# Performance work log

Measured on AMD Instinct MI355X. Metric: run time of the kernel, lower is better.

Reference implementation:

```python
import jax, jax.numpy as jnp
import numpy as np
import math

NUM_HEADS = 16
SIZE = 1024
HEAD_SIZE = SIZE // NUM_HEADS
B, S = 2, 2048


def setup_inputs() -> dict:
    key = jax.random.key(0)
    ks = jax.random.split(key, 11)
    sc = 1.0 / math.sqrt(SIZE)
    inp = {
        "q": jax.random.normal(ks[0], (B, S, SIZE), dtype=jnp.float32),
        "k": jax.random.normal(ks[1], (B, S, SIZE), dtype=jnp.float32),
        "v": jax.random.normal(ks[2], (B, S, SIZE), dtype=jnp.float32),
        "Wq": jax.random.normal(ks[3], (SIZE, SIZE), dtype=jnp.float32) * sc,
        "bq": jax.random.normal(ks[4], (SIZE,), dtype=jnp.float32) * sc,
        "Wk": jax.random.normal(ks[5], (SIZE, SIZE), dtype=jnp.float32) * sc,
        "bk": jax.random.normal(ks[6], (SIZE,), dtype=jnp.float32) * sc,
        "Wv": jax.random.normal(ks[7], (SIZE, SIZE), dtype=jnp.float32) * sc,
        "bv": jax.random.normal(ks[8], (SIZE,), dtype=jnp.float32) * sc,
        "Wo": jax.random.normal(ks[9], (SIZE, SIZE), dtype=jnp.float32) * sc,
        "bo": jax.random.normal(ks[10], (SIZE,), dtype=jnp.float32) * sc,
    }
    return inp


def _split_heads(x):
    # [B, S, SIZE] -> [B, H, S, D]
    b, s, _ = x.shape
    return x.reshape(b, s, NUM_HEADS, HEAD_SIZE).transpose(0, 2, 1, 3)


def reference(q, k, v, Wq, bq, Wk, bk, Wv, bv, Wo, bo):
    qh = _split_heads(q @ Wq.T + bq) / math.sqrt(HEAD_SIZE)  # [B,H,S,D]
    kh = _split_heads(k @ Wk.T + bk)
    vh = _split_heads(v @ Wv.T + bv)
    scores = jnp.einsum("bhqd,bhkd->bhqk", qh, kh)  # [B,H,S,S]
    attn = jax.nn.softmax(scores, axis=-1)
    ctx = jnp.einsum("bhqk,bhkd->bhqd", attn, vh)  # [B,H,S,D]
    ctx = ctx.transpose(0, 2, 1, 3).reshape(q.shape[0], -1, SIZE)
    return ctx @ Wo.T + bo
```

## Files before the change

### kernel.cpp

```cpp
#include <hip/hip_runtime.h>
#include <hip/hip_bf16.h>

#define SIZE 1024
#define NH 16
#define HD 64
#define BB 2
#define SS 2048
#define MROWS (BB * SS)
#define QT 256
#define NQT (SS / QT)
#define NKT ((SS / 2) / 64)

using bf16 = __hip_bfloat16;
using frag16 = __attribute__((ext_vector_type(8))) short;
using f32x4 = __attribute__((ext_vector_type(4))) float;
typedef unsigned int u32;

__device__ __forceinline__ void glds16(const bf16* g, bf16* l) {
    __builtin_amdgcn_global_load_lds(
        (const __attribute__((address_space(1))) u32*)g,
        (__attribute__((address_space(3))) u32*)l, 16, 0, 0);
}

__device__ __forceinline__ void cvt_store8(bf16* dst, const float* src) {
    float4 a = *(const float4*)src;
    float4 b = *(const float4*)(src + 4);
    bf16 t[8];
    t[0] = __float2bfloat16(a.x); t[1] = __float2bfloat16(a.y);
    t[2] = __float2bfloat16(a.z); t[3] = __float2bfloat16(a.w);
    t[4] = __float2bfloat16(b.x); t[5] = __float2bfloat16(b.y);
    t[6] = __float2bfloat16(b.z); t[7] = __float2bfloat16(b.w);
    *(uint4*)dst = *(const uint4*)t;
}

__global__ __launch_bounds__(256) void cast_kernel(
    const float* __restrict__ Wq, const float* __restrict__ Wk,
    const float* __restrict__ Wv, const float* __restrict__ Wo,
    const float* __restrict__ q, const float* __restrict__ k,
    const float* __restrict__ v,
    bf16* __restrict__ Wb, bf16* __restrict__ qb,
    bf16* __restrict__ kb, bf16* __restrict__ vb)
{
    const int z = blockIdx.z;
    const float* s; bf16* d; int n;
    switch (z) {
        case 0: s = Wq; d = Wb;                   n = SIZE * SIZE;  break;
        case 1: s = Wk; d = Wb + SIZE * SIZE;     n = SIZE * SIZE;  break;
        case 2: s = Wv; d = Wb + 2 * SIZE * SIZE; n = SIZE * SIZE;  break;
        case 3: s = Wo; d = Wb + 3 * SIZE * SIZE; n = SIZE * SIZE;  break;
        case 4: s = q;  d = qb;                   n = MROWS * SIZE; break;
        case 5: s = k;  d = kb;                   n = MROWS * SIZE; break;
        default: s = v; d = vb;                   n = MROWS * SIZE; break;
    }
    const int i = (blockIdx.x * 256 + threadIdx.x) * 8;
    if (i < n) cvt_store8(d + i, s + i);
}

__device__ __forceinline__ void gemm_body(
    const bf16* __restrict__ X, const bf16* __restrict__ W,
    const float* __restrict__ bias, bf16* __restrict__ Y, float scale, bool vt_mode)
{
    __shared__ __align__(16) bf16 smem[8704];
    bf16* As = smem;
    bf16* Bs = smem + 4096;

    const int tid = threadIdx.x;
    const int wave = tid >> 6;
    const int lane = tid & 63;
    const int lane15 = lane & 15;
    const int quad = lane >> 4;
    const int bm = blockIdx.y * 128;
    const int bn = blockIdx.x * 128;
    const int wm = (wave & 1) * 64;
    const int wn = (wave >> 1) * 64;

    f32x4 acc[4][4];
#pragma unroll
    for (int i = 0; i < 4; i++)
#pragma unroll
        for (int j = 0; j < 4; j++)
            acc[i][j] = (f32x4){0.f, 0.f, 0.f, 0.f};

    const int srow = lane >> 2;
    const int scol = (lane & 3) * 8;

    for (int kt = 0; kt < SIZE / 32; kt++) {
        const int k0 = kt * 32;
        __syncthreads();
#pragma unroll
        for (int n = 0; n < 2; n++) {
            const int c = wave * 2 + n;
            glds16(X + (size_t)(bm + c * 16 + srow) * SIZE + k0 + scol, As + c * 512);
            glds16(W + (size_t)(bn + c * 16 + srow) * SIZE + k0 + scol, Bs + c * 512);
        }
        __syncthreads();

        frag16 a[4], b[4];
#pragma unroll
        for (int mi = 0; mi < 4; mi++)
            a[mi] = *(const frag16*)(As + (wm + mi * 16 + lane15) * 32 + quad * 8);
#pragma unroll
        for (int ni = 0; ni < 4; ni++)
            b[ni] = *(const frag16*)(Bs + (wn + ni * 16 + lane15) * 32 + quad * 8);
#pragma unroll
        for (int mi = 0; mi < 4; mi++)
#pragma unroll
            for (int ni = 0; ni < 4; ni++)
                acc[mi][ni] = __builtin_amdgcn_mfma_f32_16x16x32_bf16(
                    a[mi], b[ni], acc[mi][ni], 0, 0, 0);
    }

    if (!vt_mode) {
#pragma unroll
        for (int ni = 0; ni < 4; ni++) {
            const int col = bn + wn + ni * 16 + lane15;
            const float bv = bias[col];
#pragma unroll
            for (int mi = 0; mi < 4; mi++) {
                const int row = bm + wm + mi * 16 + quad * 4;
#pragma unroll
                for (int r = 0; r < 4; r++)
                    Y[(size_t)(row + r) * SIZE + col] =
                        __float2bfloat16((acc[mi][ni][r] + bv) * scale);
            }
        }
    } else {
        bf16* tr = smem;
        const int bloc = bm >> 11;
        const int s0g = bm & (SS - 1);
#pragma unroll
        for (int p = 0; p < 2; p++) {
            __syncthreads();
            if ((wave >> 1) == p) {
#pragma unroll
                for (int ni = 0; ni < 4; ni++) {
                    const int colp = ni * 16 + lane15;
                    const float bv = bias[bn + p * 64 + colp];
#pragma unroll
                    for (int mi = 0; mi < 4; mi++) {
                        const int row = wm + mi * 16 + quad * 4;
#pragma unroll
                        for (int r = 0; r < 4; r++)
                            tr[colp * 136 + row + r] =
                                __float2bfloat16(acc[mi][ni][r] + bv);
                    }
                }
            }
            __syncthreads();
            const int colp = tid >> 2;
            const int gcol = bn + p * 64 + colp;
            const int hh = gcol >> 6, dd = gcol & (HD - 1);
            bf16* dst = (bf16*)Y + ((size_t)(bloc * NH + hh) * HD + dd) * SS
                        + s0g + (tid & 3) * 32;
            const bf16* src = tr + colp * 136 + (tid & 3) * 32;
#pragma unroll
            for (int j = 0; j < 4; j++)
                *(uint4*)(dst + j * 8) = *(const uint4*)(src + j * 8);
        }
    }
}

__global__ __launch_bounds__(256) void qkv_proj_kernel(
    const bf16* __restrict__ qb, const bf16* __restrict__ kb, const bf16* __restrict__ vb,
    const bf16* __restrict__ Wb,
    const float* __restrict__ bq, const float* __restrict__ bk, const float* __restrict__ bv,
    bf16* __restrict__ qh, bf16* __restrict__ kh, bf16* __restrict__ vt)
{
    const bf16 *X, *W; const float* bi; bf16* Y; float sc; bool vm;
    if (blockIdx.z == 0)      { X = qb; W = Wb;                   bi = bq; Y = qh; sc = 0.125f; vm = false; }
    else if (blockIdx.z == 1) { X = kb; W = Wb + SIZE * SIZE;     bi = bk; Y = kh; sc = 1.0f;   vm = false; }
    else                      { X = vb; W = Wb + 2 * SIZE * SIZE; bi = bv; Y = vt; sc = 1.0f;   vm = true;  }
    gemm_body(X, W, bi, Y, sc, vm);
}

__global__ __launch_bounds__(256) void attn_kernel(
    const bf16* __restrict__ qh, const bf16* __restrict__ kh,
    const bf16* __restrict__ vt, bf16* __restrict__ po, float* __restrict__ pl)
{
    __shared__ __align__(16) bf16 Ks[2][64][72];
    __shared__ __align__(16) bf16 Vs[2][64][72];
    __shared__ __align__(16) bf16 Ps[4][64][72];

    const int tid = threadIdx.x;
    const int wave = tid >> 6;
    const int lane = tid & 63;
    const int lane15 = lane & 15;
    const int quad = lane >> 4;

    const int b = blockIdx.z, h = blockIdx.y;
    const int qt = blockIdx.x >> 1;
    const int sh = blockIdx.x & 1;
    const int q0 = qt * QT;

    const size_t baseq = (size_t)b * SS * SIZE + (size_t)h * HD;
    const size_t basev = (size_t)(b * NH + h) * HD * SS;
    const float LOG2E = 1.44269504088896340736f;
    const float OFF = 12.0f * LOG2E;

    frag16 aq[4][2];
#pragma unroll
    for (int m = 0; m < 4; m++) {
        const int qrow = q0 + wave * 64 + m * 16 + lane15;
        const bf16* qp = qh + baseq + (size_t)qrow * SIZE + quad * 8;
        aq[m][0] = *(const frag16*)(qp);
        aq[m][1] = *(const frag16*)(qp + 32);
    }

    frag16 bones;
#pragma unroll
    for (int e = 0; e < 8; e++) bones[e] = (short)0x3F80;

    f32x4 ofrag[4][4], l_frag[4];
#pragma unroll
    for (int m = 0; m < 4; m++) {
        l_frag[m] = (f32x4){0.f, 0.f, 0.f, 0.f};
#pragma unroll
        for (int dt = 0; dt < 4; dt++) ofrag[m][dt] = (f32x4){0.f, 0.f, 0.f, 0.f};
    }

    const int sr = tid >> 3;
    const int sc = (tid & 7) * 8;

    uint4 rk0, rk1, rv0, rv1;

#define ISSUE(KT)                                                              \
    {                                                                          \
        const int s0_ = sh * (SS / 2) + (KT) * 64;                             \
        rk0 = *(const uint4*)(kh + baseq + (size_t)(s0_ + sr) * SIZE + sc);    \
        rk1 = *(const uint4*)(kh + baseq + (size_t)(s0_ + sr + 32) * SIZE + sc);\
        rv0 = *(const uint4*)(vt + basev + (size_t)sr * SS + s0_ + sc);        \
        rv1 = *(const uint4*)(vt + basev + (size_t)(sr + 32) * SS + s0_ + sc); \
    }
#define COMMIT(BUF)                                                            \
    {                                                                          \
        *(uint4*)&Ks[BUF][sr][sc] = rk0; *(uint4*)&Ks[BUF][sr + 32][sc] = rk1; \
        *(uint4*)&Vs[BUF][sr][sc] = rv0; *(uint4*)&Vs[BUF][sr + 32][sc] = rv1; \
    }

    ISSUE(0); COMMIT(0);
    __syncthreads();

    for (int kt = 0; kt < NKT; kt++) {
        const int buf = kt & 1;
        if (kt + 1 < NKT) ISSUE(kt + 1);
        __builtin_amdgcn_sched_barrier(0);

        frag16 kf[4][2];
#pragma unroll
        for (int nt = 0; nt < 4; nt++) {
            kf[nt][0] = *(const frag16*)&Ks[buf][nt * 16 + lane15][quad * 8];
            kf[nt][1] = *(const frag16*)&Ks[buf][nt * 16 + lane15][32 + quad * 8];
        }
#pragma unroll
        for (int m = 0; m < 4; m++) {
#pragma unroll
            for (int nt = 0; nt < 4; nt++) {
                f32x4 c = (f32x4){0.f, 0.f, 0.f, 0.f};
                c = __builtin_amdgcn_mfma_f32_16x16x32_bf16(kf[nt][0], aq[m][0], c, 0, 0, 0);
                c = __builtin_amdgcn_mfma_f32_16x16x32_bf16(kf[nt][1], aq[m][1], c, 0, 0, 0);
                bf16 p4[4];
#pragma unroll
                for (int r = 0; r < 4; r++)
                    p4[r] = __float2bfloat16(exp2f(c[r] * LOG2E - OFF));
                *(uint2*)&Ps[wave][m * 16 + lane15][nt * 16 + quad * 4] = *(const uint2*)p4;
            }
        }
        __builtin_amdgcn_wave_barrier();

        frag16 ap[4][2];
#pragma unroll
        for (int m = 0; m < 4; m++)
#pragma unroll
            for (int c2 = 0; c2 < 2; c2++)
                ap[m][c2] = *(const frag16*)&Ps[wave][m * 16 + lane15][c2 * 32 + quad * 8];

        __builtin_amdgcn_s_setprio(1);
#pragma unroll
        for (int m = 0; m < 4; m++)
#pragma unroll
            for (int c2 = 0; c2 < 2; c2++)
                l_frag[m] = __builtin_amdgcn_mfma_f32_16x16x32_bf16(
                    ap[m][c2], bones, l_frag[m], 0, 0, 0);

#pragma unroll
        for (int dt = 0; dt < 4; dt++) {
            frag16 bv0 = *(const frag16*)&Vs[buf][dt * 16 + lane15][quad * 8];
            frag16 bv1 = *(const frag16*)&Vs[buf][dt * 16 + lane15][32 + quad * 8];
#pragma unroll
            for (int m = 0; m < 4; m++) {
                ofrag[m][dt] = __builtin_amdgcn_mfma_f32_16x16x32_bf16(ap[m][0], bv0, ofrag[m][dt], 0, 0, 0);
                ofrag[m][dt] = __builtin_amdgcn_mfma_f32_16x16x32_bf16(ap[m][1], bv1, ofrag[m][dt], 0, 0, 0);
            }
        }
        __builtin_amdgcn_s_setprio(0);

        if (kt + 1 < NKT) {
            COMMIT(buf ^ 1);
            __syncthreads();
        }
    }
#undef ISSUE
#undef COMMIT

    const int pb = ((b * NH + h) * NQT + qt) * 2 + sh;
    if (lane15 == 0) {
        float* plp = pl + (size_t)pb * QT;
#pragma unroll
        for (int m = 0; m < 4; m++)
#pragma unroll
            for (int r = 0; r < 4; r++)
                plp[wave * 64 + m * 16 + quad * 4 + r] = l_frag[m][r];
    }
    bf16* pop = po + (size_t)pb * QT * HD;
#pragma unroll
    for (int m = 0; m < 4; m++)
#pragma unroll
        for (int dt = 0; dt < 4; dt++)
#pragma unroll
            for (int r = 0; r < 4; r++)
                pop[(size_t)(wave * 64 + m * 16 + quad * 4 + r) * HD + dt * 16 + lane15] =
                    __float2bfloat16(ofrag[m][dt][r]);
}

__global__ __launch_bounds__(256) void combine_kernel(
    const bf16* __restrict__ po, const float* __restrict__ pl, bf16* __restrict__ ctx)
{
    const int b = blockIdx.z, h = blockIdx.y, qt = blockIdx.x;
    const int t = (b * NH + h) * NQT + (qt >> 1);
    const int rbase = (qt & 1) * 128;
    const bf16* p0 = po + (size_t)(t * 2 + 0) * QT * HD;
    const bf16* p1 = po + (size_t)(t * 2 + 1) * QT * HD;
    const int qr = threadIdx.x >> 1;
    const int dh = (threadIdx.x & 1) * 32;
    const int row = rbase + qr;
    const float l = pl[(size_t)(t * 2) * QT + row] + pl[(size_t)(t * 2 + 1) * QT + row];
    const float inv = 1.0f / fmaxf(l, 1e-30f);
    bf16* dst = ctx + ((size_t)b * SS + qt * 128 + qr) * SIZE + h * HD + dh;
    const bf16* s0p = p0 + row * HD + dh;
    const bf16* s1p = p1 + row * HD + dh;
#pragma unroll
    for (int j = 0; j < 32; j += 8) {
        uint4 u0 = *(const uint4*)(s0p + j);
        uint4 u1 = *(const uint4*)(s1p + j);
        const bf16* a = (const bf16*)&u0;
        const bf16* bt = (const bf16*)&u1;
        bf16 o[8];
#pragma unroll
        for (int e = 0; e < 8; e++)
            o[e] = __float2bfloat16((__bfloat162float(a[e]) + __bfloat162float(bt[e])) * inv);
        *(uint4*)(dst + j) = *(const uint4*)o;
    }
}

__global__ __launch_bounds__(256) void out_proj_kernel(
    const bf16* __restrict__ ctx, const bf16* __restrict__ Wob,
    const float* __restrict__ bo, float* __restrict__ out)
{
    __shared__ __align__(16) bf16 As[64 * 32];
    __shared__ __align__(16) bf16 Bs[128 * 32];

    const int tid = threadIdx.x;
    const int wave = tid >> 6;
    const int lane = tid & 63;
    const int lane15 = lane & 15;
    const int quad = lane >> 4;
    const int bm = blockIdx.y * 64;
    const int bn = blockIdx.x * 128;
    const int wn = wave * 32;

    f32x4 acc[4][2];
#pragma unroll
    for (int i = 0; i < 4; i++)
#pragma unroll
        for (int j = 0; j < 2; j++)
            acc[i][j] = (f32x4){0.f, 0.f, 0.f, 0.f};

    const int srow = lane >> 2;
    const int scol = (lane & 3) * 8;

    for (int kt = 0; kt < SIZE / 32; kt++) {
        const int k0 = kt * 32;
        __syncthreads();
        glds16(ctx + (size_t)(bm + wave * 16 + srow) * SIZE + k0 + scol, As + wave * 512);
#pragma unroll
        for (int n = 0; n < 2; n++) {
            const int c = wave * 2 + n;
            glds16(Wob + (size_t)(bn + c * 16 + srow) * SIZE + k0 + scol, Bs + c * 512);
        }
        __syncthreads();

        frag16 a[4], b[2];
#pragma unroll
        for (int mi = 0; mi < 4; mi++)
            a[mi] = *(const frag16*)(As + (mi * 16 + lane15) * 32 + quad * 8);
#pragma unroll
        for (int ni = 0; ni < 2; ni++)
            b[ni] = *(const frag16*)(Bs + (wn + ni * 16 + lane15) * 32 + quad * 8);
#pragma unroll
        for (int mi = 0; mi < 4; mi++)
#pragma unroll
            for (int ni = 0; ni < 2; ni++)
                acc[mi][ni] = __builtin_amdgcn_mfma_f32_16x16x32_bf16(
                    a[mi], b[ni], acc[mi][ni], 0, 0, 0);
    }

#pragma unroll
    for (int ni = 0; ni < 2; ni++) {
        const int col = bn + wn + ni * 16 + lane15;
        const float bv = bo[col];
#pragma unroll
        for (int mi = 0; mi < 4; mi++) {
            const int row = bm + mi * 16 + quad * 4;
#pragma unroll
            for (int r = 0; r < 4; r++)
                out[(size_t)(row + r) * SIZE + col] = acc[mi][ni][r] + bv;
        }
    }
}

extern "C" void kernel_launch(void* const* d_in, const int* in_sizes, int n_in,
                              void* d_out, int out_size, void* d_ws, size_t ws_size,
                              hipStream_t stream) {
    const float* q  = (const float*)d_in[0];
    const float* k  = (const float*)d_in[1];
    const float* v  = (const float*)d_in[2];
    const float* Wq = (const float*)d_in[3];
    const float* bq = (const float*)d_in[4];
    const float* Wk = (const float*)d_in[5];
    const float* bk = (const float*)d_in[6];
    const float* Wv = (const float*)d_in[7];
    const float* bv = (const float*)d_in[8];
    const float* Wo = (const float*)d_in[9];
    const float* bo = (const float*)d_in[10];
    float* out = (float*)d_out;

    bf16* Wb  = (bf16*)d_ws;
    bf16* qb  = Wb + (size_t)4 * SIZE * SIZE;
    bf16* kb  = qb + (size_t)MROWS * SIZE;
    bf16* vb  = kb + (size_t)MROWS * SIZE;
    bf16* qh  = vb + (size_t)MROWS * SIZE;
    bf16* kh  = qh + (size_t)MROWS * SIZE;
    bf16* vt  = kh + (size_t)MROWS * SIZE;
    bf16* po  = qb;
    bf16* ctx = vb;
    float* pl = (float*)Wb;

    cast_kernel<<<dim3(MROWS * SIZE / 2048, 1, 7), 256, 0, stream>>>(
        Wq, Wk, Wv, Wo, q, k, v, Wb, qb, kb, vb);
    qkv_proj_kernel<<<dim3(SIZE / 128, MROWS / 128, 3), 256, 0, stream>>>(
        qb, kb, vb, Wb, bq, bk, bv, qh, kh, vt);
    attn_kernel<<<dim3(NQT * 2, NH, BB), 256, 0, stream>>>(qh, kh, vt, po, pl);
    combine_kernel<<<dim3(SS / 128, NH, BB), 256, 0, stream>>>(po, pl, ctx);
    out_proj_kernel<<<dim3(SIZE / 128, MROWS / 64, 1), 256, 0, stream>>>(
        ctx, Wb + (size_t)3 * SIZE * SIZE, bo, out);
}
```

Before: 252.9 us.

## Fuse partial-softmax combine into out-proj, deepen GEMM K tile, flatten cast grid

Removes the separate combine kernel. The out-projection now reads the two partial attention outputs and their normalisers directly, merges and normalises them in registers, and writes the A tile to shared memory, prefetching the next head's data during the MFMA work. The QKV and out-proj GEMMs step through K 64 at a time with doubled LDS buffers, halving barrier count. The cast kernel uses a flat grid so most blocks no longer sit idle. The cost is that each of the 8 column blocks redoes the combine for the same rows, repeating that work and its global reads, and LDS use per block grows.

```diff
diff --git a/kernel.cpp b/kernel.cpp
--- a/kernel.cpp
+++ b/kernel.cpp
@@ -41,28 +41,31 @@
     bf16* __restrict__ Wb, bf16* __restrict__ qb,
     bf16* __restrict__ kb, bf16* __restrict__ vb)
 {
-    const int z = blockIdx.z;
-    const float* s; bf16* d; int n;
-    switch (z) {
-        case 0: s = Wq; d = Wb;                   n = SIZE * SIZE;  break;
-        case 1: s = Wk; d = Wb + SIZE * SIZE;     n = SIZE * SIZE;  break;
-        case 2: s = Wv; d = Wb + 2 * SIZE * SIZE; n = SIZE * SIZE;  break;
-        case 3: s = Wo; d = Wb + 3 * SIZE * SIZE; n = SIZE * SIZE;  break;
-        case 4: s = q;  d = qb;                   n = MROWS * SIZE; break;
-        case 5: s = k;  d = kb;                   n = MROWS * SIZE; break;
-        default: s = v; d = vb;                   n = MROWS * SIZE; break;
-    }
-    const int i = (blockIdx.x * 256 + threadIdx.x) * 8;
-    if (i < n) cvt_store8(d + i, s + i);
+    const size_t WN = (size_t)SIZE * SIZE;
+    const size_t AN = (size_t)MROWS * SIZE;
+    const size_t e = ((size_t)blockIdx.x * 256 + threadIdx.x) * 8;
+    if (e < 4 * WN) {
+        const int which = (int)(e >> 20);
+        const size_t off = e & (WN - 1);
+        const float* s = (which == 0) ? Wq : (which == 1) ? Wk : (which == 2) ? Wv : Wo;
+        cvt_store8(Wb + e, s + off);
+    } else {
+        const size_t a = e - 4 * WN;
+        const int which = (int)(a >> 22);
+        const size_t off = a & (AN - 1);
+        const float* s = (which == 0) ? q : (which == 1) ? k : v;
+        bf16* d = (which == 0) ? qb : (which == 1) ? kb : vb;
+        cvt_store8(d + off, s + off);
+    }
 }
 
 __device__ __forceinline__ void gemm_body(
     const bf16* __restrict__ X, const bf16* __restrict__ W,
     const float* __restrict__ bias, bf16* __restrict__ Y, float scale, bool vt_mode)
 {
-    __shared__ __align__(16) bf16 smem[8704];
+    __shared__ __align__(16) bf16 smem[16384];
     bf16* As = smem;
-    bf16* Bs = smem + 4096;
+    bf16* Bs = smem + 8192;
 
     const int tid = threadIdx.x;
     const int wave = tid >> 6;
@@ -84,30 +87,37 @@
     const int srow = lane >> 2;
     const int scol = (lane & 3) * 8;
 
-    for (int kt = 0; kt < SIZE / 32; kt++) {
-        const int k0 = kt * 32;
+    for (int kt = 0; kt < SIZE / 64; kt++) {
+        const int k0 = kt * 64;
         __syncthreads();
 #pragma unroll
-        for (int n = 0; n < 2; n++) {
-            const int c = wave * 2 + n;
-            glds16(X + (size_t)(bm + c * 16 + srow) * SIZE + k0 + scol, As + c * 512);
-            glds16(W + (size_t)(bn + c * 16 + srow) * SIZE + k0 + scol, Bs + c * 512);
+        for (int n = 0; n < 4; n++) {
+            const int c = wave * 4 + n;
+            const int plane = c >> 3;
+            const int cc = c & 7;
+            glds16(X + (size_t)(bm + cc * 16 + srow) * SIZE + k0 + plane * 32 + scol,
+                   As + c * 512);
+            glds16(W + (size_t)(bn + cc * 16 + srow) * SIZE + k0 + plane * 32 + scol,
+                   Bs + c * 512);
         }
         __syncthreads();
 
-        frag16 a[4], b[4];
-#pragma unroll
-        for (int mi = 0; mi < 4; mi++)
-            a[mi] = *(const frag16*)(As + (wm + mi * 16 + lane15) * 32 + quad * 8);
-#pragma unroll
-        for (int ni = 0; ni < 4; ni++)
-            b[ni] = *(const frag16*)(Bs + (wn + ni * 16 + lane15) * 32 + quad * 8);
-#pragma unroll
-        for (int mi = 0; mi < 4; mi++)
+#pragma unroll
+        for (int kk = 0; kk < 2; kk++) {
+            frag16 a[4], b[4];
+#pragma unroll
+            for (int mi = 0; mi < 4; mi++)
+                a[mi] = *(const frag16*)(As + kk * 4096 + (wm + mi * 16 + lane15) * 32 + quad * 8);
 #pragma unroll
             for (int ni = 0; ni < 4; ni++)
-                acc[mi][ni] = __builtin_amdgcn_mfma_f32_16x16x32_bf16(
-                    a[mi], b[ni], acc[mi][ni], 0, 0, 0);
+                b[ni] = *(const frag16*)(Bs + kk * 4096 + (wn + ni * 16 + lane15) * 32 + quad * 8);
+#pragma unroll
+            for (int mi = 0; mi < 4; mi++)
+#pragma unroll
+                for (int ni = 0; ni < 4; ni++)
+                    acc[mi][ni] = __builtin_amdgcn_mfma_f32_16x16x32_bf16(
+                        a[mi], b[ni], acc[mi][ni], 0, 0, 0);
+        }
     }
 
     if (!vt_mode) {
@@ -322,42 +332,13 @@
                     __float2bfloat16(ofrag[m][dt][r]);
 }
 
-__global__ __launch_bounds__(256) void combine_kernel(
-    const bf16* __restrict__ po, const float* __restrict__ pl, bf16* __restrict__ ctx)
+__global__ __launch_bounds__(256) void out_proj_kernel(
+    const bf16* __restrict__ po, const float* __restrict__ pl,
+    const bf16* __restrict__ Wob, const float* __restrict__ bo,
+    float* __restrict__ out)
 {
-    const int b = blockIdx.z, h = blockIdx.y, qt = blockIdx.x;
-    const int t = (b * NH + h) * NQT + (qt >> 1);
-    const int rbase = (qt & 1) * 128;
-    const bf16* p0 = po + (size_t)(t * 2 + 0) * QT * HD;
-    const bf16* p1 = po + (size_t)(t * 2 + 1) * QT * HD;
-    const int qr = threadIdx.x >> 1;
-    const int dh = (threadIdx.x & 1) * 32;
-    const int row = rbase + qr;
-    const float l = pl[(size_t)(t * 2) * QT + row] + pl[(size_t)(t * 2 + 1) * QT + row];
-    const float inv = 1.0f / fmaxf(l, 1e-30f);
-    bf16* dst = ctx + ((size_t)b * SS + qt * 128 + qr) * SIZE + h * HD + dh;
-    const bf16* s0p = p0 + row * HD + dh;
-    const bf16* s1p = p1 + row * HD + dh;
-#pragma unroll
-    for (int j = 0; j < 32; j += 8) {
-        uint4 u0 = *(const uint4*)(s0p + j);
-        uint4 u1 = *(const uint4*)(s1p + j);
-        const bf16* a = (const bf16*)&u0;
-        const bf16* bt = (const bf16*)&u1;
-        bf16 o[8];
-#pragma unroll
-        for (int e = 0; e < 8; e++)
-            o[e] = __float2bfloat16((__bfloat162float(a[e]) + __bfloat162float(bt[e])) * inv);
-        *(uint4*)(dst + j) = *(const uint4*)o;
-    }
-}
-
-__global__ __launch_bounds__(256) void out_proj_kernel(
-    const bf16* __restrict__ ctx, const bf16* __restrict__ Wob,
-    const float* __restrict__ bo, float* __restrict__ out)
-{
-    __shared__ __align__(16) bf16 As[64 * 32];
-    __shared__ __align__(16) bf16 Bs[128 * 32];
+    __shared__ __align__(16) bf16 As[2 * 64 * 32];
+    __shared__ __align__(16) bf16 Bs[2 * 128 * 32];
 
     const int tid = threadIdx.x;
     const int wave = tid >> 6;
@@ -378,31 +359,77 @@
     const int srow = lane >> 2;
     const int scol = (lane & 3) * 8;
 
-    for (int kt = 0; kt < SIZE / 32; kt++) {
-        const int k0 = kt * 32;
+    const int arow = tid >> 2;
+    const int acol = (tid & 3) * 8;
+    const int gr = bm + arow;
+    const int bIdx = gr >> 11;
+    const int s = gr & (SS - 1);
+    const int qt8 = s >> 8;
+    const int sq = s & (QT - 1);
+
+    uint4 p0a, p1a, p0b, p1b;
+    float l0, l1;
+
+#define ALOAD(KT)                                                                 \
+    {                                                                             \
+        const int pb0_ = ((bIdx * NH + (KT)) * NQT + qt8) * 2;                    \
+        const bf16* q0_ = po + (size_t)pb0_ * QT * HD + sq * HD;                  \
+        const bf16* q1_ = po + (size_t)(pb0_ + 1) * QT * HD + sq * HD;            \
+        p0a = *(const uint4*)(q0_ + acol);                                        \
+        p0b = *(const uint4*)(q0_ + 32 + acol);                                   \
+        p1a = *(const uint4*)(q1_ + acol);                                        \
+        p1b = *(const uint4*)(q1_ + 32 + acol);                                   \
+        l0 = pl[(size_t)pb0_ * QT + sq];                                          \
+        l1 = pl[(size_t)(pb0_ + 1) * QT + sq];                                    \
+    }
+
+    ALOAD(0);
+
+    for (int kt = 0; kt < NH; kt++) {
         __syncthreads();
-        glds16(ctx + (size_t)(bm + wave * 16 + srow) * SIZE + k0 + scol, As + wave * 512);
-#pragma unroll
-        for (int n = 0; n < 2; n++) {
-            const int c = wave * 2 + n;
-            glds16(Wob + (size_t)(bn + c * 16 + srow) * SIZE + k0 + scol, Bs + c * 512);
+        {
+            const float inv = 1.0f / fmaxf(l0 + l1, 1e-30f);
+            const bf16* x0 = (const bf16*)&p0a; const bf16* y0 = (const bf16*)&p1a;
+            const bf16* x1 = (const bf16*)&p0b; const bf16* y1 = (const bf16*)&p1b;
+            bf16 o0[8], o1[8];
+#pragma unroll
+            for (int e = 0; e < 8; e++) {
+                o0[e] = __float2bfloat16((__bfloat162float(x0[e]) + __bfloat162float(y0[e])) * inv);
+                o1[e] = __float2bfloat16((__bfloat162float(x1[e]) + __bfloat162float(y1[e])) * inv);
+            }
+            *(uint4*)(As + 0 * 2048 + arow * 32 + acol) = *(const uint4*)o0;
+            *(uint4*)(As + 1 * 2048 + arow * 32 + acol) = *(const uint4*)o1;
+        }
+#pragma unroll
+        for (int n = 0; n < 4; n++) {
+            const int c = wave * 4 + n;
+            const int plane = c >> 3;
+            const int cc = c & 7;
+            glds16(Wob + (size_t)(bn + cc * 16 + srow) * SIZE + kt * 64 + plane * 32 + scol,
+                   Bs + c * 512);
         }
         __syncthreads();
 
-        frag16 a[4], b[2];
-#pragma unroll
-        for (int mi = 0; mi < 4; mi++)
-            a[mi] = *(const frag16*)(As + (mi * 16 + lane15) * 32 + quad * 8);
-#pragma unroll
-        for (int ni = 0; ni < 2; ni++)
-            b[ni] = *(const frag16*)(Bs + (wn + ni * 16 + lane15) * 32 + quad * 8);
-#pragma unroll
-        for (int mi = 0; mi < 4; mi++)
+        if (kt + 1 < NH) ALOAD(kt + 1);
+
+#pragma unroll
+        for (int kk = 0; kk < 2; kk++) {
+            frag16 a[4], b[2];
+#pragma unroll
+            for (int mi = 0; mi < 4; mi++)
+                a[mi] = *(const frag16*)(As + kk * 2048 + (mi * 16 + lane15) * 32 + quad * 8);
 #pragma unroll
             for (int ni = 0; ni < 2; ni++)
-                acc[mi][ni] = __builtin_amdgcn_mfma_f32_16x16x32_bf16(
-                    a[mi], b[ni], acc[mi][ni], 0, 0, 0);
-    }
+                b[ni] = *(const frag16*)(Bs + kk * 4096 + (wn + ni * 16 + lane15) * 32 + quad * 8);
+#pragma unroll
+            for (int mi = 0; mi < 4; mi++)
+#pragma unroll
+                for (int ni = 0; ni < 2; ni++)
+                    acc[mi][ni] = __builtin_amdgcn_mfma_f32_16x16x32_bf16(
+                        a[mi], b[ni], acc[mi][ni], 0, 0, 0);
+        }
+    }
+#undef ALOAD
 
 #pragma unroll
     for (int ni = 0; ni < 2; ni++) {
@@ -442,15 +469,13 @@
     bf16* kh  = qh + (size_t)MROWS * SIZE;
     bf16* vt  = kh + (size_t)MROWS * SIZE;
     bf16* po  = qb;
-    bf16* ctx = vb;
     float* pl = (float*)Wb;
 
-    cast_kernel<<<dim3(MROWS * SIZE / 2048, 1, 7), 256, 0, stream>>>(
+    cast_kernel<<<dim3(8192, 1, 1), 256, 0, stream>>>(
         Wq, Wk, Wv, Wo, q, k, v, Wb, qb, kb, vb);
     qkv_proj_kernel<<<dim3(SIZE / 128, MROWS / 128, 3), 256, 0, stream>>>(
         qb, kb, vb, Wb, bq, bk, bv, qh, kh, vt);
     attn_kernel<<<dim3(NQT * 2, NH, BB), 256, 0, stream>>>(qh, kh, vt, po, pl);
-    combine_kernel<<<dim3(SS / 128, NH, BB), 256, 0, stream>>>(po, pl, ctx);
     out_proj_kernel<<<dim3(SIZE / 128, MROWS / 64, 1), 256, 0, stream>>>(
-        ctx, Wb + (size_t)3 * SIZE * SIZE, bo, out);
-}
+        po, pl, Wb + (size_t)3 * SIZE * SIZE, bo, out);
+}
```

New measurement: 254.5 us. No clear change (+0.7%).
